# Kernel tuning notes

Hardware: AMD Instinct MI355X
Metric: run time of the kernel (lower is better)

The kernel has to match this reference:

```python
import jax, jax.numpy as jnp
import numpy as np

N, E, VD, HD, ES = 10000, 80000, 32, 64, 68
NET_IN = VD * VD + 2 * HD + ES   # 1220: f2s(1024) + s[e0](64) + s[e1](64) + edge_s(68)
SELF_IN = VD * VD + 2 * HD       # 1152: temp_f2s(1024) + s(64) + s_c(64)
OUT_D = VD * VD + HD             # 1088: vector channel mixer + scalar update


def _lecun(k, fin, fout):
    return jax.random.normal(k, (fin, fout), jnp.float32) / jnp.sqrt(jnp.float32(fin))


def setup_inputs() -> dict:
    ks = jax.random.split(jax.random.key(0), 16)
    return {
        "f": jax.random.normal(ks[0], (N, 3, VD), jnp.float32),
        "s": jax.random.normal(ks[1], (N, HD), jnp.float32),
        "edge_f": jax.random.normal(ks[2], (E, 3, 1), jnp.float32),
        "edge_s": jax.random.normal(ks[3], (E, ES), jnp.float32),
        "W_emb1": _lecun(ks[4], 2 * VD + 1, VD),
        "net_W1": _lecun(ks[5], NET_IN, HD), "net_b1": jnp.zeros((HD,), jnp.float32),
        "net_W2": _lecun(ks[6], HD, HD), "net_b2": jnp.zeros((HD,), jnp.float32),
        "net_W3": _lecun(ks[7], HD, OUT_D), "net_b3": jnp.zeros((OUT_D,), jnp.float32),
        "W_emb2": _lecun(ks[8], 2 * VD, VD),
        "self_W1": _lecun(ks[9], SELF_IN, HD), "self_b1": jnp.zeros((HD,), jnp.float32),
        "self_W2": _lecun(ks[10], HD, HD), "self_b2": jnp.zeros((HD,), jnp.float32),
        "self_W3": _lecun(ks[11], HD, OUT_D), "self_b3": jnp.zeros((OUT_D,), jnp.float32),
        "edge_index": jax.random.randint(ks[12], (2, E), 0, N),
    }


def _mlp(x, W1, b1, W2, b2, W3, b3):
    h = jax.nn.relu(x @ W1 + b1)
    h = jax.nn.relu(h @ W2 + b2)
    return h @ W3 + b3


def _segment_mean(x, ids, n):
    tot = jax.ops.segment_sum(x, ids, num_segments=n)
    cnt = jax.ops.segment_sum(jnp.ones(ids.shape, x.dtype), ids, num_segments=n)
    return tot / jnp.maximum(cnt, 1.0).reshape((n,) + (1,) * (x.ndim - 1))


def _forward(f, s, edge_f, edge_s,
             W_emb1, net_W1, net_b1, net_W2, net_b2, net_W3, net_b3,
             W_emb2, self_W1, self_b1, self_W2, self_b2, self_W3, self_b3,
             edge_index):
    n = f.shape[0]
    e0, e1 = edge_index[0], edge_index[1]
    # --- edge message: gather -> embed -> gram einsum -> MLP ---
    _f = jnp.concatenate((f[e0], f[e1], edge_f), axis=-1)          # [E,3,2VD+1]
    _s = jnp.concatenate((s[e0], s[e1], edge_s), axis=-1)          # [E,2HD+ES]
    _f = _f @ W_emb1                                               # [E,3,VD]
    f2s = jnp.einsum('eij,eik->ejk', _f, _f).reshape(-1, VD * VD)  # _f^T @ _f, [E,VD*VD]
    Fn = jnp.linalg.norm(f2s, axis=-1, keepdims=True) + 1.0
    c = _mlp(jnp.concatenate((f2s, _s), axis=-1),
             net_W1, net_b1, net_W2, net_b2, net_W3, net_b3) / Fn  # [E,OUT_D]
    f_c = jnp.einsum('eij,ejk->eik', _f, c[:, :VD * VD].reshape(-1, VD, VD))  # [E,3,VD]
    f_c = _segment_mean(f_c, e0, n)                                # [N,3,VD]
    s_c = _segment_mean(c[:, VD * VD:], e0, n)                     # [N,HD]
    # --- node self-update ---
    tf = jnp.concatenate((f, f_c), axis=-1) @ W_emb2               # [N,3,VD]
    tf2s = jnp.einsum('nij,nik->njk', tf, tf).reshape(n, VD * VD)
    Fn2 = jnp.linalg.norm(tf2s, axis=-1, keepdims=True) + 1.0
    c2 = _mlp(jnp.concatenate((tf2s, s, s_c), axis=-1),
              self_W1, self_b1, self_W2, self_b2, self_W3, self_b3) / Fn2
    f_out = jnp.einsum('nij,njk->nik', tf, c2[:, :VD * VD].reshape(-1, VD, VD)) + f
    s_out = c2[:, VD * VD:] + s
    return f_out, s_out


def reference(f, s, edge_f, edge_s,
              W_emb1, net_W1, net_b1, net_W2, net_b2, net_W3, net_b3,
              W_emb2, self_W1, self_b1, self_W2, self_b2, self_W3, self_b3,
              edge_index):
    return _forward(f, s, edge_f, edge_s,
                    W_emb1, net_W1, net_b1, net_W2, net_b2, net_W3, net_b3,
                    W_emb2, self_W1, self_b1, self_W2, self_b2, self_W3, self_b3,
                    edge_index)
```

## Files before the change

kernel.cpp:

```cpp
#include <hip/hip_runtime.h>
#include <math.h>

#define NN 10000
#define NE 80000
#define SFH 102
#define SFB 98
#define SSB 66
#define STX 72
#define NTRI 528
#define SAE 104
#define SAN 72

typedef __attribute__((ext_vector_type(8))) __bf16 bf16x8;
typedef __attribute__((ext_vector_type(8))) short short8v;
typedef __attribute__((ext_vector_type(4))) float f32x4;
typedef __attribute__((ext_vector_type(4))) unsigned uint4v;

__device__ __forceinline__ ushort f2bf(float x) {
  union { float f; unsigned u; } v; v.f = x;
  unsigned r = v.u + 0x7FFFu + ((v.u >> 16) & 1u);
  return (ushort)(r >> 16);
}
__device__ __forceinline__ float bfu(ushort u) {
  union { unsigned x; float f; } v; v.x = (unsigned)u << 16;
  return v.f;
}
__device__ __forceinline__ void tri_ab(int k, int& a, int& b) {
  int aa = 0, rem = k;
  while (rem >= 32 - aa) { rem -= 32 - aa; ++aa; }
  a = aa; b = aa + rem;
}

__global__ __launch_bounds__(1024)
void sgnn_scan(const int* __restrict__ deg, int* __restrict__ cursor,
               int* __restrict__ start) {
  __shared__ int sm[1024];
  const int t = threadIdx.x;
  const int i0 = t * 10;
  int v[10], pre = 0;
  #pragma unroll
  for (int q = 0; q < 10; ++q) {
    const int i = i0 + q;
    v[q] = (i < NN) ? deg[i] : 0;
    pre += v[q];
  }
  sm[t] = pre;
  __syncthreads();
  int run = pre;
  #pragma unroll
  for (int d = 1; d < 1024; d <<= 1) {
    const int add = (t >= d) ? sm[t - d] : 0;
    __syncthreads();
    run += add;
    sm[t] = run;
    __syncthreads();
  }
  int excl = run - pre;
  #pragma unroll
  for (int q = 0; q < 10; ++q) {
    const int i = i0 + q;
    if (i < NN) { cursor[i] = excl; start[i] = excl; }
    excl += v[q];
  }
}

__global__ __launch_bounds__(256)
void sgnn_scatter(const int* __restrict__ eidx, int* __restrict__ cursor,
                  int* __restrict__ sorted) {
  const int e = blockIdx.x * 256 + threadIdx.x;
  if (e < NE) {
    const int p = atomicAdd(cursor + eidx[e], 1);
    sorted[p] = e;
  }
}

__global__ __launch_bounds__(256)
void sgnn_wconv(const float* __restrict__ nW1, const float* __restrict__ nW2,
                const float* __restrict__ nW3, const float* __restrict__ sW1,
                const float* __restrict__ sW2, const float* __restrict__ sW3,
                const float* __restrict__ Wemb1, const float* __restrict__ Wemb2,
                const int* __restrict__ eidx, int* __restrict__ deg,
                ushort* __restrict__ wout, ushort* __restrict__ tab) {
  const int gid = blockIdx.x * 256 + threadIdx.x;
  if (gid < NE) atomicAdd(deg + eidx[gid], 1);
  if (gid >= 61 * 4096) {
    const int k = gid - 61 * 4096;
    if (k < NTRI) {
      int a, b; tri_ab(k, a, b);
      tab[k] = (ushort)(a | (b << 8) | ((a != b) ? 0x8000 : 0));
    }
    return;
  }
  const int tile = gid >> 12, idx = gid & 4095;
  const int c = idx >> 6, k = idx & 63;
  float v = 0.f;
  if (tile < 12) {
    const int T = tile;
    if (T < 8 || (T == 8 && k < 16)) {
      const int ktri = T * 64 + k;
      if (ktri < NTRI) {
        int a, b; tri_ab(ktri, a, b);
        v = nW1[(a * 32 + b) * 64 + c];
        if (a != b) v += nW1[(b * 32 + a) * 64 + c];
      }
    } else if (T == 8) { if (k < 20) v = nW1[(1216 + (k - 16)) * 64 + c]; }
    else if (T == 9)   v = nW1[(1024 + k) * 64 + c];
    else if (T == 10)  v = nW1[(1088 + k) * 64 + c];
    else               v = nW1[(1152 + k) * 64 + c];
  } else if (tile == 12) v = nW2[k * 64 + c];
  else if (tile < 30)    v = nW3[k * 1088 + (tile - 13) * 64 + c];
  else if (tile < 41) {
    const int T = tile - 30;
    if (T < 8 || (T == 8 && k < 16)) {
      const int ktri = T * 64 + k;
      if (ktri < NTRI) {
        int a, b; tri_ab(ktri, a, b);
        v = sW1[(a * 32 + b) * 64 + c];
        if (a != b) v += sW1[(b * 32 + a) * 64 + c];
      }
    } else if (T == 9) v = sW1[(1024 + k) * 64 + c];
    else if (T == 10)  v = sW1[(1088 + k) * 64 + c];
  } else if (tile == 41) v = sW2[k * 64 + c];
  else if (tile < 59)    v = sW3[k * 1088 + (tile - 42) * 64 + c];
  else if (tile == 59) {
    const int col = idx / 96, kk = idx % 96;
    v = (col < 32 && kk < 65) ? Wemb1[kk * 32 + col] : 0.f;
  } else {
    const int col = idx >> 6;
    v = (col < 32) ? Wemb2[k * 32 + col] : 0.f;
  }
  wout[gid] = f2bf(v);
}

#define WPRE_LOAD(srcbase) do { const ushort* _s = (srcbase);                    \
  wpre0 = *(const short8v*)&_s[(t >> 3) * 64 + (t & 7) * 8];                     \
  wpre1 = *(const short8v*)&_s[(32 + (t >> 3)) * 64 + (t & 7) * 8]; } while (0)

#define WPRE_STORE_TO(Wd) do { ushort* _d = (Wd);                                \
  *(short8v*)&_d[(t >> 3) * STX + (t & 7) * 8] = wpre0;                          \
  *(short8v*)&_d[(32 + (t >> 3)) * STX + (t & 7) * 8] = wpre1; } while (0)

#define MFMA_K64_RA_B(Wb) do { const ushort* _wl = (Wb);                         \
  acc[0] = __builtin_amdgcn_mfma_f32_16x16x32_bf16(af0.v8,                       \
      *(const bf16x8*)&_wl[(     ll) * STX + lh * 8], acc[0], 0, 0, 0);          \
  acc[1] = __builtin_amdgcn_mfma_f32_16x16x32_bf16(af0.v8,                       \
      *(const bf16x8*)&_wl[(16 + ll) * STX + lh * 8], acc[1], 0, 0, 0);          \
  acc[2] = __builtin_amdgcn_mfma_f32_16x16x32_bf16(af0.v8,                       \
      *(const bf16x8*)&_wl[(32 + ll) * STX + lh * 8], acc[2], 0, 0, 0);          \
  acc[3] = __builtin_amdgcn_mfma_f32_16x16x32_bf16(af0.v8,                       \
      *(const bf16x8*)&_wl[(48 + ll) * STX + lh * 8], acc[3], 0, 0, 0);          \
  acc[0] = __builtin_amdgcn_mfma_f32_16x16x32_bf16(af1.v8,                       \
      *(const bf16x8*)&_wl[(     ll) * STX + 32 + lh * 8], acc[0], 0, 0, 0);     \
  acc[1] = __builtin_amdgcn_mfma_f32_16x16x32_bf16(af1.v8,                       \
      *(const bf16x8*)&_wl[(16 + ll) * STX + 32 + lh * 8], acc[1], 0, 0, 0);     \
  acc[2] = __builtin_amdgcn_mfma_f32_16x16x32_bf16(af1.v8,                       \
      *(const bf16x8*)&_wl[(32 + ll) * STX + 32 + lh * 8], acc[2], 0, 0, 0);     \
  acc[3] = __builtin_amdgcn_mfma_f32_16x16x32_bf16(af1.v8,                       \
      *(const bf16x8*)&_wl[(48 + ll) * STX + 32 + lh * 8], acc[3], 0, 0, 0);     \
} while (0)

#define MFMA_K64_B(Xb, Wb) do { const ushort* _x = (Xb); const ushort* _wl = (Wb);\
  _Pragma("unroll") for (int kb = 0; kb < 2; ++kb) {                             \
    const bf16x8 af_ = *(const bf16x8*)&_x[(w * 16 + ll) * STX + kb * 32 + lh * 8]; \
    acc[0] = __builtin_amdgcn_mfma_f32_16x16x32_bf16(af_,                        \
        *(const bf16x8*)&_wl[(     ll) * STX + kb * 32 + lh * 8], acc[0], 0, 0, 0); \
    acc[1] = __builtin_amdgcn_mfma_f32_16x16x32_bf16(af_,                        \
        *(const bf16x8*)&_wl[(16 + ll) * STX + kb * 32 + lh * 8], acc[1], 0, 0, 0); \
    acc[2] = __builtin_amdgcn_mfma_f32_16x16x32_bf16(af_,                        \
        *(const bf16x8*)&_wl[(32 + ll) * STX + kb * 32 + lh * 8], acc[2], 0, 0, 0); \
    acc[3] = __builtin_amdgcn_mfma_f32_16x16x32_bf16(af_,                        \
        *(const bf16x8*)&_wl[(48 + ll) * STX + kb * 32 + lh * 8], acc[3], 0, 0, 0); \
  } } while (0)

#define ZERO_ACC() do { _Pragma("unroll") for (int q = 0; q < 4; ++q)            \
    acc[q] = (f32x4){0.f, 0.f, 0.f, 0.f}; } while (0)

#define PACK_STORE16(dstp) do {                                                  \
  unsigned pk[8];                                                                \
  _Pragma("unroll") for (int q = 0; q < 8; ++q)                                  \
    pk[q] = (unsigned)f2bf(xv[2 * q]) | ((unsigned)f2bf(xv[2 * q + 1]) << 16);   \
  *(uint4v*)(dstp)       = (uint4v){pk[0], pk[1], pk[2], pk[3]};                 \
  *(uint4v*)((dstp) + 8) = (uint4v){pk[4], pk[5], pk[6], pk[7]};                 \
} while (0)

#define PACK_AF() do {                                                           \
  _Pragma("unroll") for (int q2 = 0; q2 < 4; ++q2) {                             \
    af0.u[q2] = (unsigned)f2bf(xv[2 * q2]) | ((unsigned)f2bf(xv[2 * q2 + 1]) << 16); \
    af1.u[q2] = (unsigned)f2bf(xv[8 + 2 * q2]) | ((unsigned)f2bf(xv[8 + 2 * q2 + 1]) << 16); \
  } } while (0)

#define TRI8(kt, off) do {                                                       \
  int prev_a = -1; float fa0 = 0.f, fa1 = 0.f, fa2 = 0.f;                        \
  _Pragma("unroll") for (int q = 0; q < 8; ++q) {                                \
    const int tb = tabL[(kt) + q];                                               \
    const int a_ = tb & 31, b_ = (tb >> 8) & 31;                                 \
    if (a_ != prev_a) { fa0 = bfu(frA[a_]); fa1 = bfu(frA[32 + a_]);             \
                        fa2 = bfu(frA[64 + a_]); prev_a = a_; }                  \
    const float v = fmaf(fa0, bfu(frA[b_]),                                      \
        fmaf(fa1, bfu(frA[32 + b_]), fa2 * bfu(frA[64 + b_])));                  \
    const float wsel = (tb & 0x8000) ? 2.f : 1.f;                                \
    sumsq = fmaf(v * wsel, v, sumsq);                                            \
    xv[(off) + q] = v;                                                           \
  } } while (0)

#define XV8_LOAD(p, off) do { const float* _p = (p);                             \
  const float4 va = *(const float4*)(_p);                                        \
  const float4 vb = *(const float4*)(_p + 4);                                    \
  xv[(off)+0]=va.x; xv[(off)+1]=va.y; xv[(off)+2]=va.z; xv[(off)+3]=va.w;        \
  xv[(off)+4]=vb.x; xv[(off)+5]=vb.y; xv[(off)+6]=vb.z; xv[(off)+7]=vb.w;        \
} while (0)

#define XV_LOAD16(p) do { const float* _p = (p);                                 \
  _Pragma("unroll") for (int q = 0; q < 4; ++q) {                                \
    const float4 v4 = *(const float4*)(_p + 4 * q);                              \
    xv[4 * q + 0] = v4.x; xv[4 * q + 1] = v4.y;                                  \
    xv[4 * q + 2] = v4.z; xv[4 * q + 3] = v4.w; } } while (0)

#define CONSUME_NT() do {                                                        \
  _Pragma("unroll") for (int r = 0; r < 4; ++r) {                                \
    const int row_ = w * 16 + lh * 4 + r;                                        \
    const unsigned u0 = *(const unsigned*)&smFh[row_ * SFH +      nt * 2];       \
    const unsigned u1 = *(const unsigned*)&smFh[row_ * SFH + 32 + nt * 2];       \
    const unsigned u2 = *(const unsigned*)&smFh[row_ * SFH + 64 + nt * 2];       \
    union { unsigned x; float f; } l0, h0, l1, h1, l2, h2;                       \
    l0.x = u0 << 16; h0.x = u0 & 0xffff0000u;                                    \
    l1.x = u1 << 16; h1.x = u1 & 0xffff0000u;                                    \
    l2.x = u2 << 16; h2.x = u2 & 0xffff0000u;                                    \
    _Pragma("unroll") for (int nc = 0; nc < 4; ++nc) {                           \
      const float cv = (acc[nc][r] + b3v[nc]) * ifnr[r];                         \
      const int p = nc & 1;                                                      \
      const float f0 = (nc < 2) ? l0.f : h0.f;                                   \
      const float f1 = (nc < 2) ? l1.f : h1.f;                                   \
      const float f2 = (nc < 2) ? l2.f : h2.f;                                   \
      fch[(r * 3 + 0) * 2 + p] = fmaf(f0, cv, fch[(r * 3 + 0) * 2 + p]);         \
      fch[(r * 3 + 1) * 2 + p] = fmaf(f1, cv, fch[(r * 3 + 1) * 2 + p]);         \
      fch[(r * 3 + 2) * 2 + p] = fmaf(f2, cv, fch[(r * 3 + 2) * 2 + p]);         \
    }                                                                            \
  } } while (0)

#define STAGE_FS() do {                                                          \
  _Pragma("unroll") for (int r = 0; r < 4; ++r) {                                \
    const int row_ = w * 16 + lh * 4 + r;                                        \
    _Pragma("unroll") for (int i = 0; i < 3; ++i) {                              \
      F[row_ * SFB + i * 32 + ll]      = f2bf(fch[(r * 3 + i) * 2 + 0]);         \
      F[row_ * SFB + i * 32 + ll + 16] = f2bf(fch[(r * 3 + i) * 2 + 1]);         \
    }                                                                            \
    _Pragma("unroll") for (int nc = 0; nc < 4; ++nc)                             \
      S[row_ * SSB + nc * 16 + ll] = f2bf(cs[nc * 4 + r]);                       \
  } } while (0)

#define LDS_BYTES 43872

__global__ __launch_bounds__(256, 3)
void sgnn_edge(const float* __restrict__ f, const float* __restrict__ s,
               const float* __restrict__ edge_f, const float* __restrict__ edge_s,
               const float* __restrict__ b1, const float* __restrict__ b2,
               const float* __restrict__ b3,
               const ushort* __restrict__ wbf, const ushort* __restrict__ tab_g,
               const int* __restrict__ eidx, const int* __restrict__ sorted,
               const int* __restrict__ start_g, const int* __restrict__ deg_g,
               float* __restrict__ fc_sum, float* __restrict__ sc_sum) {
  __shared__ __align__(16) char sbuf[LDS_BYTES];
  ushort* smFh = (ushort*)sbuf;
  ushort* F    = (ushort*)sbuf;
  ushort* Xl   = (ushort*)(sbuf + 13056);
  ushort* S    = (ushort*)(sbuf + 13056);
  ushort* Aemb = (ushort*)(sbuf + 13056);
  ushort* Wl   = (ushort*)(sbuf + 22272);
  int*    snode = (int*)(sbuf + 31488);
  int*    srow0 = snode + 8;
  int*    srow1 = snode + 16;
  int*    sst   = snode + 24;
  int*    sdg   = snode + 32;
  ushort* tabL = (ushort*)(sbuf + 33088);
  float*  iFn  = (float*)(sbuf + 33088);
  int*    es_s = (int*)(sbuf + 34144);
  ushort* e0s  = (ushort*)(sbuf + 34400);
  ushort* e1s  = (ushort*)(sbuf + 34528);
  ushort* Wl1  = (ushort*)(sbuf + 34656);

  const int t = threadIdx.x, j = t & 63, w = t >> 6, eb = w * 16;
  const int lh = j >> 4, ll = j & 15;
  const int bid = blockIdx.x;
  const ushort* wembT = wbf + 59 * 4096;
  short8v wpre0, wpre1;

  if (t < 64) {
    const int e = sorted[bid * 64 + t];
    es_s[t] = e;
    e0s[t] = (ushort)eidx[e];
    e1s[t] = (ushort)eidx[NE + e];
  }
  for (int idx = t; idx < NTRI; idx += 256) tabL[idx] = tab_g[idx];
  __syncthreads();

  int str = 0, dgr = 0;
  if (j < 16) {
    const int n_ = e0s[eb + j];
    str = start_g[n_];
    dgr = deg_g[n_];
  }
  WPRE_LOAD(wbf + 0);

  #pragma unroll 1
  for (int h = 0; h < 2; ++h) {
    const int hb = h * 32;
    #pragma unroll 1
    for (int cc = t; cc < 576; cc += 256) {
      const int row = cc / 6, seg = cc - row * 6;
      const int lel = (row * 43) >> 7, il = row - lel * 3;
      const int k0 = seg * 16;
      float xv[16];
      if (seg < 4) {
        const int nd = (seg < 2) ? (int)e0s[hb + lel] : (int)e1s[hb + lel];
        XV_LOAD16(f + nd * 96 + il * 32 + (seg & 1) * 16);
      } else if (seg == 4) {
        xv[0] = edge_f[es_s[hb + lel] * 3 + il];
        #pragma unroll
        for (int m = 1; m < 16; ++m) xv[m] = 0.f;
      } else {
        #pragma unroll
        for (int m = 0; m < 16; ++m) xv[m] = 0.f;
      }
      PACK_STORE16(&Aemb[row * SAE + k0]);
    }
    __syncthreads();
    #pragma unroll 1
    for (int job = w * 3; job < w * 3 + 3; ++job) {
      const int mt = job >> 1, nt = job & 1;
      f32x4 ac = (f32x4){0.f, 0.f, 0.f, 0.f};
      #pragma unroll
      for (int kb = 0; kb < 3; ++kb) {
        const bf16x8 av = *(const bf16x8*)&Aemb[(mt * 16 + ll) * SAE + kb * 32 + lh * 8];
        const bf16x8 bv = *(const bf16x8*)&wembT[(nt * 16 + ll) * 96 + kb * 32 + lh * 8];
        ac = __builtin_amdgcn_mfma_f32_16x16x32_bf16(av, bv, ac, 0, 0, 0);
      }
      #pragma unroll
      for (int r = 0; r < 4; ++r) {
        const int rr = mt * 16 + lh * 4 + r;
        const int lel = (rr * 43) >> 7, il = rr - lel * 3;
        smFh[(hb + lel) * SFH + il * 32 + nt * 16 + ll] = f2bf(ac[r]);
      }
    }
    __syncthreads();
  }

  f32x4 acc[4];
  ZERO_ACC();
  float sumsq = 0.f;
  const int rowA = w * 16 + ll;
  const ushort* frA = smFh + rowA * SFH;

  WPRE_STORE_TO(Wl);
  WPRE_LOAD(wbf + 1 * 4096);
  __syncthreads();
  #pragma unroll 1
  for (int T = 0; T < 12; ++T) {
    ushort* Wc = (T & 1) ? Xl : Wl;
    ushort* Wn = (T & 1) ? Wl : Xl;
    float xv[16];
    union { unsigned u[4]; bf16x8 v8; } af0, af1;
    if (T < 8) {
      TRI8(T * 64 + lh * 8, 0);
      TRI8(T * 64 + 32 + lh * 8, 8);
    } else if (T == 8) {
      #pragma unroll
      for (int kb2 = 0; kb2 < 2; ++kb2)
        #pragma unroll
        for (int q = 0; q < 8; ++q) {
          const int k = kb2 * 32 + lh * 8 + q;
          float v = 0.f;
          if (k < 16) {
            const int tb = tabL[512 + k];
            const int a_ = tb & 31, b_ = (tb >> 8) & 31;
            v = fmaf(bfu(frA[a_]), bfu(frA[b_]),
                fmaf(bfu(frA[32 + a_]), bfu(frA[32 + b_]),
                     bfu(frA[64 + a_]) * bfu(frA[64 + b_])));
            const float wsel = (tb & 0x8000) ? 2.f : 1.f;
            sumsq = fmaf(v * wsel, v, sumsq);
          } else if (k < 20) {
            v = edge_s[es_s[rowA] * 68 + 64 + (k - 16)];
          }
          xv[kb2 * 8 + q] = v;
        }
    } else {
      const float* p = (T == 9)  ? (s + e0s[rowA] * 64)
                     : (T == 10) ? (s + e1s[rowA] * 64)
                                 : (edge_s + es_s[rowA] * 68);
      XV8_LOAD(p + lh * 8, 0);
      XV8_LOAD(p + 32 + lh * 8, 8);
    }
    PACK_AF();
    WPRE_STORE_TO(Wn);
    WPRE_LOAD(wbf + (T + 2) * 4096);
    MFMA_K64_RA_B(Wc);
    __syncthreads();
  }

  {
    float ss = sumsq;
    ss += __shfl_xor(ss, 16);
    ss += __shfl_xor(ss, 32);
    if (j < 16) iFn[eb + j] = 1.f / (sqrtf(ss) + 1.f);
  }
  #pragma unroll
  for (int nc = 0; nc < 4; ++nc) {
    const float bv = b1[nc * 16 + ll];
    #pragma unroll
    for (int r = 0; r < 4; ++r)
      Xl[(w * 16 + lh * 4 + r) * STX + nc * 16 + ll] = f2bf(fmaxf(acc[nc][r] + bv, 0.f));
  }
  ZERO_ACC();
  MFMA_K64_B(Xl, Wl);
  #pragma unroll
  for (int nc = 0; nc < 4; ++nc) {
    const float bv = b2[nc * 16 + ll];
    #pragma unroll
    for (int r = 0; r < 4; ++r)
      Xl[(w * 16 + lh * 4 + r) * STX + nc * 16 + ll] = f2bf(fmaxf(acc[nc][r] + bv, 0.f));
  }
  WPRE_STORE_TO(Wl1);
  WPRE_LOAD(wbf + 14 * 4096);
  __syncthreads();

  float fch[24];
  #pragma unroll
  for (int q = 0; q < 24; ++q) fch[q] = 0.f;
  float cs[16];
  float ifnr[4];
  #pragma unroll
  for (int r = 0; r < 4; ++r) ifnr[r] = iFn[w * 16 + lh * 4 + r];

  #pragma unroll 1
  for (int nt = 0; nt < 17; ++nt) {
    ushort* Wc = (nt & 1) ? Wl : Wl1;
    ushort* Wn = (nt & 1) ? Wl1 : Wl;
    if (nt < 16) {
      WPRE_STORE_TO(Wn);
      if (nt < 15) WPRE_LOAD(wbf + (15 + nt) * 4096);
    }
    float b3v[4];
    #pragma unroll
    for (int nc = 0; nc < 4; ++nc) b3v[nc] = b3[nt * 64 + nc * 16 + ll];
    ZERO_ACC();
    MFMA_K64_B(Xl, Wc);
    if (nt < 16) {
      CONSUME_NT();
    } else {
      #pragma unroll
      for (int nc = 0; nc < 4; ++nc)
        #pragma unroll
        for (int r = 0; r < 4; ++r)
          cs[nc * 4 + r] = (acc[nc][r] + b3v[nc]) * ifnr[r];
    }
    __syncthreads();
  }

  STAGE_FS();
  if (t < 8) snode[t] = -1;
  __syncthreads();

  {
    float r0 = 0.f, r1 = 0.f, rs = 0.f;
    int runlen = 0;
    const int gwb = bid * 64 + eb;
    #pragma unroll 1
    for (int m = 0; m < 16; ++m) {
      const int row = eb + m;
      r0 += bfu(F[row * SFB + j]);
      if (j < 32) r1 += bfu(F[row * SFB + 64 + j]);
      rs += bfu(S[row * SSB + j]);
      ++runlen;
      const int n = e0s[row];
      if (m == 15 || e0s[row + 1] != n) {
        const int st = __shfl(str, m);
        const int dg = __shfl(dgr, m);
        const int g1v = gwb + m, g0v = g1v - runlen + 1;
        if (g0v == st && runlen == dg) {
          fc_sum[n * 96 + j] = r0;
          if (j < 32) fc_sum[n * 96 + 64 + j] = r1;
          sc_sum[n * 64 + j] = rs;
        } else {
          const int slot = (g0v == gwb) ? 2 * w : 2 * w + 1;
          if (j == 0) {
            snode[slot] = n; srow0[slot] = row - runlen + 1; srow1[slot] = row;
            sst[slot] = st; sdg[slot] = dg;
          }
        }
        r0 = r1 = rs = 0.f; runlen = 0;
      }
    }
  }
  __syncthreads();

  if (t < 160) {
    const int ch = t;
    int prevn = -1;
    #pragma unroll 1
    for (int ss = 0; ss < 8; ++ss) {
      const int n = snode[ss];
      if (n < 0) continue;
      if (n != prevn) {
        float v = 0.f;
        #pragma unroll 1
        for (int k2 = ss; k2 < 8; ++k2) {
          if (snode[k2] == n) {
            #pragma unroll 1
            for (int row = srow0[k2]; row <= srow1[k2]; ++row)
              v += (ch < 96) ? bfu(F[row * SFB + ch]) : bfu(S[row * SSB + (ch - 96)]);
          } else if (k2 > ss && snode[k2] >= 0) break;
        }
        const bool cib = (sst[ss] >= bid * 64) && (sst[ss] + sdg[ss] <= bid * 64 + 64);
        float* dst = (ch < 96) ? (fc_sum + n * 96 + ch) : (sc_sum + n * 64 + (ch - 96));
        if (cib) *dst = v; else atomicAdd(dst, v);
      }
      prevn = n;
    }
  }
}

__global__ __launch_bounds__(256, 3)
void sgnn_node(const float* __restrict__ f, const float* __restrict__ s,
               const float* __restrict__ b1, const float* __restrict__ b2,
               const float* __restrict__ b3,
               const ushort* __restrict__ wbf, const ushort* __restrict__ tab_g,
               const float* __restrict__ fcm, const float* __restrict__ scm,
               const int* __restrict__ deg_g,
               float* __restrict__ of, float* __restrict__ os) {
  __shared__ __align__(16) char sbuf[LDS_BYTES];
  ushort* smFh = (ushort*)sbuf;
  ushort* F    = (ushort*)sbuf;
  ushort* Xl   = (ushort*)(sbuf + 13056);
  ushort* S    = (ushort*)(sbuf + 13056);
  ushort* Aemb = (ushort*)(sbuf + 13056);
  ushort* Wl   = (ushort*)(sbuf + 22272);
  float*  icntL = (float*)(sbuf + 31488);
  ushort* tabL = (ushort*)(sbuf + 33088);
  float*  iFn  = (float*)(sbuf + 33088);
  ushort* Wl1  = (ushort*)(sbuf + 34656);

  const int t = threadIdx.x, j = t & 63, w = t >> 6, eb = w * 16;
  const int lh = j >> 4, ll = j & 15;
  const int nbase = blockIdx.x * 64;
  const ushort* wembTn = wbf + 60 * 4096;
  short8v wpre0, wpre1;

  for (int idx = t; idx < NTRI; idx += 256) tabL[idx] = tab_g[idx];
  if (t < 64)
    icntL[t] = 1.f / fmaxf((float)deg_g[min(nbase + t, NN - 1)], 1.f);
  WPRE_LOAD(wbf + 30 * 4096);
  __syncthreads();

  #pragma unroll 1
  for (int h = 0; h < 2; ++h) {
    const int hb = h * 32;
    #pragma unroll 1
    for (int cc = t; cc < 384; cc += 256) {
      const int row = cc >> 2, seg = cc & 3;
      const int lel = (row * 43) >> 7, il = row - lel * 3;
      const int nc = min(nbase + hb + lel, NN - 1);
      const int k0 = seg * 16;
      float xv[16];
      if (seg < 2) {
        XV_LOAD16(f + nc * 96 + il * 32 + seg * 16);
      } else {
        XV_LOAD16(fcm + nc * 96 + il * 32 + (seg - 2) * 16);
        const float ic = icntL[hb + lel];
        #pragma unroll
        for (int m = 0; m < 16; ++m) xv[m] *= ic;
      }
      PACK_STORE16(&Aemb[row * SAN + k0]);
    }
    __syncthreads();
    #pragma unroll 1
    for (int job = w * 3; job < w * 3 + 3; ++job) {
      const int mt = job >> 1, nt = job & 1;
      f32x4 ac = (f32x4){0.f, 0.f, 0.f, 0.f};
      #pragma unroll
      for (int kb = 0; kb < 2; ++kb) {
        const bf16x8 av = *(const bf16x8*)&Aemb[(mt * 16 + ll) * SAN + kb * 32 + lh * 8];
        const bf16x8 bv = *(const bf16x8*)&wembTn[(nt * 16 + ll) * 64 + kb * 32 + lh * 8];
        ac = __builtin_amdgcn_mfma_f32_16x16x32_bf16(av, bv, ac, 0, 0, 0);
      }
      #pragma unroll
      for (int r = 0; r < 4; ++r) {
        const int rr = mt * 16 + lh * 4 + r;
        const int lel = (rr * 43) >> 7, il = rr - lel * 3;
        smFh[(hb + lel) * SFH + il * 32 + nt * 16 + ll] = f2bf(ac[r]);
      }
    }
    __syncthreads();
  }

  f32x4 acc[4];
  ZERO_ACC();
  float sumsq = 0.f;
  const int rowA = w * 16 + ll;
  const ushort* frA = smFh + rowA * SFH;
  const int ncA = min(nbase + rowA, NN - 1);

  WPRE_STORE_TO(Xl);
  WPRE_LOAD(wbf + 31 * 4096);
  __syncthreads();
  #pragma unroll 1
  for (int T = 0; T < 11; ++T) {
    ushort* Wc = (T & 1) ? Wl : Xl;
    ushort* Wn = (T & 1) ? Xl : Wl;
    float xv[16];
    union { unsigned u[4]; bf16x8 v8; } af0, af1;
    if (T < 8) {
      TRI8(T * 64 + lh * 8, 0);
      TRI8(T * 64 + 32 + lh * 8, 8);
    } else if (T == 8) {
      #pragma unroll
      for (int kb2 = 0; kb2 < 2; ++kb2)
        #pragma unroll
        for (int q = 0; q < 8; ++q) {
          const int k = kb2 * 32 + lh * 8 + q;
          float v = 0.f;
          if (k < 16) {
            const int tb = tabL[512 + k];
            const int a_ = tb & 31, b_ = (tb >> 8) & 31;
            v = fmaf(bfu(frA[a_]), bfu(frA[b_]),
                fmaf(bfu(frA[32 + a_]), bfu(frA[32 + b_]),
                     bfu(frA[64 + a_]) * bfu(frA[64 + b_])));
            const float wsel = (tb & 0x8000) ? 2.f : 1.f;
            sumsq = fmaf(v * wsel, v, sumsq);
          }
          xv[kb2 * 8 + q] = v;
        }
    } else if (T == 9) {
      XV8_LOAD(s + ncA * 64 + lh * 8, 0);
      XV8_LOAD(s + ncA * 64 + 32 + lh * 8, 8);
    } else {
      const float ic = icntL[rowA];
      XV8_LOAD(scm + ncA * 64 + lh * 8, 0);
      XV8_LOAD(scm + ncA * 64 + 32 + lh * 8, 8);
      #pragma unroll
      for (int m = 0; m < 16; ++m) xv[m] *= ic;
    }
    PACK_AF();
    WPRE_STORE_TO(Wn);
    WPRE_LOAD(wbf + (32 + T) * 4096);
    MFMA_K64_RA_B(Wc);
    __syncthreads();
  }

  {
    float ss = sumsq;
    ss += __shfl_xor(ss, 16);
    ss += __shfl_xor(ss, 32);
    if (j < 16) iFn[eb + j] = 1.f / (sqrtf(ss) + 1.f);
  }
  #pragma unroll
  for (int nc = 0; nc < 4; ++nc) {
    const float bv = b1[nc * 16 + ll];
    #pragma unroll
    for (int r = 0; r < 4; ++r)
      Xl[(w * 16 + lh * 4 + r) * STX + nc * 16 + ll] = f2bf(fmaxf(acc[nc][r] + bv, 0.f));
  }
  ZERO_ACC();
  MFMA_K64_B(Xl, Wl);
  #pragma unroll
  for (int nc = 0; nc < 4; ++nc) {
    const float bv = b2[nc * 16 + ll];
    #pragma unroll
    for (int r = 0; r < 4; ++r)
      Xl[(w * 16 + lh * 4 + r) * STX + nc * 16 + ll] = f2bf(fmaxf(acc[nc][r] + bv, 0.f));
  }
  WPRE_STORE_TO(Wl1);
  WPRE_LOAD(wbf + 43 * 4096);
  __syncthreads();

  float fch[24];
  #pragma unroll
  for (int q = 0; q < 24; ++q) fch[q] = 0.f;
  float cs[16];
  float ifnr[4];
  #pragma unroll
  for (int r = 0; r < 4; ++r) ifnr[r] = iFn[w * 16 + lh * 4 + r];

  #pragma unroll 1
  for (int nt = 0; nt < 17; ++nt) {
    ushort* Wc = (nt & 1) ? Wl : Wl1;
    ushort* Wn = (nt & 1) ? Wl1 : Wl;
    if (nt < 16) {
      WPRE_STORE_TO(Wn);
      if (nt < 15) WPRE_LOAD(wbf + (44 + nt) * 4096);
    }
    float b3v[4];
    #pragma unroll
    for (int nc = 0; nc < 4; ++nc) b3v[nc] = b3[nt * 64 + nc * 16 + ll];
    ZERO_ACC();
    MFMA_K64_B(Xl, Wc);
    if (nt < 16) {
      CONSUME_NT();
    } else {
      #pragma unroll
      for (int nc = 0; nc < 4; ++nc)
        #pragma unroll
        for (int r = 0; r < 4; ++r)
          cs[nc * 4 + r] = (acc[nc][r] + b3v[nc]) * ifnr[r];
    }
    __syncthreads();
  }

  STAGE_FS();
  __syncthreads();

  #pragma unroll 1
  for (int m = 0; m < 16; ++m) {
    const int row = eb + m;
    const int n_m = nbase + row;
    if (n_m < NN) {
      of[n_m * 96 + j] = bfu(F[row * SFB + j]) + f[n_m * 96 + j];
      if (j < 32)
        of[n_m * 96 + 64 + j] = bfu(F[row * SFB + 64 + j]) + f[n_m * 96 + 64 + j];
      os[n_m * 64 + j] = bfu(S[row * SSB + j]) + s[n_m * 64 + j];
    }
  }
}

extern "C" void kernel_launch(void* const* d_in, const int* in_sizes, int n_in,
                              void* d_out, int out_size, void* d_ws, size_t ws_size,
                              hipStream_t stream) {
  const float* f      = (const float*)d_in[0];
  const float* s      = (const float*)d_in[1];
  const float* edge_f = (const float*)d_in[2];
  const float* edge_s = (const float*)d_in[3];
  const float* Wemb1  = (const float*)d_in[4];
  const float* nW1 = (const float*)d_in[5];
  const float* nb1 = (const float*)d_in[6];
  const float* nW2 = (const float*)d_in[7];
  const float* nb2 = (const float*)d_in[8];
  const float* nW3 = (const float*)d_in[9];
  const float* nb3 = (const float*)d_in[10];
  const float* Wemb2 = (const float*)d_in[11];
  const float* sW1 = (const float*)d_in[12];
  const float* sb1 = (const float*)d_in[13];
  const float* sW2 = (const float*)d_in[14];
  const float* sb2 = (const float*)d_in[15];
  const float* sW3 = (const float*)d_in[16];
  const float* sb3 = (const float*)d_in[17];
  const int* eidx  = (const int*)d_in[18];

  float* of = (float*)d_out;
  float* os = of + (size_t)NN * 96;

  int* deg    = (int*)d_ws;
  int* cursor = deg + NN;
  int* start  = cursor + NN;
  int* sorted = start + NN;
  ushort* wbf = (ushort*)(sorted + NE);
  ushort* tab = wbf + 61 * 4096;

  hipMemsetAsync(deg, 0, (size_t)NN * 4, stream);
  hipMemsetAsync(d_out, 0, (size_t)NN * 160 * 4, stream);

  hipLaunchKernelGGL(sgnn_wconv, dim3((61 * 4096 + NTRI + 255) / 256), dim3(256),
                     0, stream, nW1, nW2, nW3, sW1, sW2, sW3, Wemb1, Wemb2,
                     eidx, deg, wbf, tab);
  hipLaunchKernelGGL(sgnn_scan, dim3(1), dim3(1024), 0, stream, deg, cursor, start);
  hipLaunchKernelGGL(sgnn_scatter, dim3((NE + 255) / 256), dim3(256), 0, stream,
                     eidx, cursor, sorted);
  hipLaunchKernelGGL(sgnn_edge, dim3(NE / 64), dim3(256), 0, stream,
                     f, s, edge_f, edge_s, nb1, nb2, nb3,
                     wbf, tab, eidx, sorted, start, deg,
                     of , os );
  hipLaunchKernelGGL(sgnn_node, dim3((NN + 63) / 64), dim3(256), 0, stream,
                     f, s, sb1, sb2, sb3,
                     wbf, tab, of , os , deg, of, os);
}
```

Baseline: 195.1 us.

## Shrink node kernel blocks to 32 nodes with 128 threads

The node-update kernel now handles 32 nodes per block with 2 waves instead of 64 nodes with 4 waves. This doubles the grid to about 313 blocks so more CUs get work, and roughly halves LDS per block. Weight staging changes from register prefetch one tile ahead to direct global-to-LDS copies into double-buffered LDS. In exchange, each weight tile is loaded by twice as many blocks, and the load latency is no longer hidden behind the previous tile's MFMA work.

```diff
diff --git a/kernel.cpp b/kernel.cpp
--- a/kernel.cpp
+++ b/kernel.cpp
@@ -140,6 +140,12 @@
   *(short8v*)&_d[(t >> 3) * STX + (t & 7) * 8] = wpre0;                          \
   *(short8v*)&_d[(32 + (t >> 3)) * STX + (t & 7) * 8] = wpre1; } while (0)
 
+#define NSTAGE_W(Wd, srcbase) do { ushort* _d = (Wd); const ushort* _s = (srcbase);\
+  _Pragma("unroll") for (int rr = 0; rr < 4; ++rr) {                             \
+    const int idx_ = t + 128 * rr; const int c_ = idx_ >> 3, ko_ = idx_ & 7;     \
+    *(short8v*)&_d[c_ * STX + ko_ * 8] = *(const short8v*)&_s[c_ * 64 + ko_ * 8];\
+  } } while (0)
+
 #define MFMA_K64_RA_B(Wb) do { const ushort* _wl = (Wb);                         \
   acc[0] = __builtin_amdgcn_mfma_f32_16x16x32_bf16(af0.v8,                       \
       *(const bf16x8*)&_wl[(     ll) * STX + lh * 8], acc[0], 0, 0, 0);          \
@@ -519,7 +525,9 @@
   }
 }
 
-__global__ __launch_bounds__(256, 3)
+#define NLDS_BYTES 30752
+
+__global__ __launch_bounds__(128, 2)
 void sgnn_node(const float* __restrict__ f, const float* __restrict__ s,
                const float* __restrict__ b1, const float* __restrict__ b2,
                const float* __restrict__ b3,
@@ -527,70 +535,64 @@
                const float* __restrict__ fcm, const float* __restrict__ scm,
                const int* __restrict__ deg_g,
                float* __restrict__ of, float* __restrict__ os) {
-  __shared__ __align__(16) char sbuf[LDS_BYTES];
+  __shared__ __align__(16) char sbuf[NLDS_BYTES];
   ushort* smFh = (ushort*)sbuf;
   ushort* F    = (ushort*)sbuf;
-  ushort* Xl   = (ushort*)(sbuf + 13056);
-  ushort* S    = (ushort*)(sbuf + 13056);
-  ushort* Aemb = (ushort*)(sbuf + 13056);
-  ushort* Wl   = (ushort*)(sbuf + 22272);
-  float*  icntL = (float*)(sbuf + 31488);
-  ushort* tabL = (ushort*)(sbuf + 33088);
-  float*  iFn  = (float*)(sbuf + 33088);
-  ushort* Wl1  = (ushort*)(sbuf + 34656);
+  ushort* Xl   = (ushort*)(sbuf + 6528);
+  ushort* S    = (ushort*)(sbuf + 6528);
+  ushort* Aemb = (ushort*)(sbuf + 6528);
+  ushort* Wl   = (ushort*)(sbuf + 11136);
+  ushort* Wl1  = (ushort*)(sbuf + 20352);
+  float*  icntL = (float*)(sbuf + 29568);
+  ushort* tabL = (ushort*)(sbuf + 29696);
+  float*  iFn  = (float*)(sbuf + 29696);
 
   const int t = threadIdx.x, j = t & 63, w = t >> 6, eb = w * 16;
   const int lh = j >> 4, ll = j & 15;
-  const int nbase = blockIdx.x * 64;
+  const int nbase = blockIdx.x * 32;
   const ushort* wembTn = wbf + 60 * 4096;
-  short8v wpre0, wpre1;
-
-  for (int idx = t; idx < NTRI; idx += 256) tabL[idx] = tab_g[idx];
-  if (t < 64)
+
+  for (int idx = t; idx < NTRI; idx += 128) tabL[idx] = tab_g[idx];
+  if (t < 32)
     icntL[t] = 1.f / fmaxf((float)deg_g[min(nbase + t, NN - 1)], 1.f);
-  WPRE_LOAD(wbf + 30 * 4096);
   __syncthreads();
 
   #pragma unroll 1
-  for (int h = 0; h < 2; ++h) {
-    const int hb = h * 32;
-    #pragma unroll 1
-    for (int cc = t; cc < 384; cc += 256) {
-      const int row = cc >> 2, seg = cc & 3;
-      const int lel = (row * 43) >> 7, il = row - lel * 3;
-      const int nc = min(nbase + hb + lel, NN - 1);
-      const int k0 = seg * 16;
-      float xv[16];
-      if (seg < 2) {
-        XV_LOAD16(f + nc * 96 + il * 32 + seg * 16);
-      } else {
-        XV_LOAD16(fcm + nc * 96 + il * 32 + (seg - 2) * 16);
-        const float ic = icntL[hb + lel];
-        #pragma unroll
-        for (int m = 0; m < 16; ++m) xv[m] *= ic;
-      }
-      PACK_STORE16(&Aemb[row * SAN + k0]);
-    }
-    __syncthreads();
-    #pragma unroll 1
-    for (int job = w * 3; job < w * 3 + 3; ++job) {
-      const int mt = job >> 1, nt = job & 1;
-      f32x4 ac = (f32x4){0.f, 0.f, 0.f, 0.f};
+  for (int cc = t; cc < 384; cc += 128) {
+    const int row = cc >> 2, seg = cc & 3;
+    const int lel = (row * 43) >> 7, il = row - lel * 3;
+    const int nc = min(nbase + lel, NN - 1);
+    const int k0 = seg * 16;
+    float xv[16];
+    if (seg < 2) {
+      XV_LOAD16(f + nc * 96 + il * 32 + seg * 16);
+    } else {
+      XV_LOAD16(fcm + nc * 96 + il * 32 + (seg - 2) * 16);
+      const float ic = icntL[lel];
       #pragma unroll
-      for (int kb = 0; kb < 2; ++kb) {
-        const bf16x8 av = *(const bf16x8*)&Aemb[(mt * 16 + ll) * SAN + kb * 32 + lh * 8];
-        const bf16x8 bv = *(const bf16x8*)&wembTn[(nt * 16 + ll) * 64 + kb * 32 + lh * 8];
-        ac = __builtin_amdgcn_mfma_f32_16x16x32_bf16(av, bv, ac, 0, 0, 0);
-      }
-      #pragma unroll
-      for (int r = 0; r < 4; ++r) {
-        const int rr = mt * 16 + lh * 4 + r;
-        const int lel = (rr * 43) >> 7, il = rr - lel * 3;
-        smFh[(hb + lel) * SFH + il * 32 + nt * 16 + ll] = f2bf(ac[r]);
-      }
-    }
-    __syncthreads();
-  }
+      for (int m = 0; m < 16; ++m) xv[m] *= ic;
+    }
+    PACK_STORE16(&Aemb[row * SAN + k0]);
+  }
+  __syncthreads();
+  #pragma unroll 1
+  for (int job = w * 6; job < w * 6 + 6; ++job) {
+    const int mt = job >> 1, nt = job & 1;
+    f32x4 ac = (f32x4){0.f, 0.f, 0.f, 0.f};
+    #pragma unroll
+    for (int kb = 0; kb < 2; ++kb) {
+      const bf16x8 av = *(const bf16x8*)&Aemb[(mt * 16 + ll) * SAN + kb * 32 + lh * 8];
+      const bf16x8 bv = *(const bf16x8*)&wembTn[(nt * 16 + ll) * 64 + kb * 32 + lh * 8];
+      ac = __builtin_amdgcn_mfma_f32_16x16x32_bf16(av, bv, ac, 0, 0, 0);
+    }
+    #pragma unroll
+    for (int r = 0; r < 4; ++r) {
+      const int rr = mt * 16 + lh * 4 + r;
+      const int lel = (rr * 43) >> 7, il = rr - lel * 3;
+      smFh[lel * SFH + il * 32 + nt * 16 + ll] = f2bf(ac[r]);
+    }
+  }
+  __syncthreads();
 
   f32x4 acc[4];
   ZERO_ACC();
@@ -599,13 +601,12 @@
   const ushort* frA = smFh + rowA * SFH;
   const int ncA = min(nbase + rowA, NN - 1);
 
-  WPRE_STORE_TO(Xl);
-  WPRE_LOAD(wbf + 31 * 4096);
+  NSTAGE_W(Wl, wbf + 30 * 4096);
   __syncthreads();
   #pragma unroll 1
   for (int T = 0; T < 11; ++T) {
-    ushort* Wc = (T & 1) ? Wl : Xl;
-    ushort* Wn = (T & 1) ? Xl : Wl;
+    ushort* Wc = (T & 1) ? Wl1 : Wl;
+    ushort* Wn = (T & 1) ? Wl : Wl1;
     float xv[16];
     union { unsigned u[4]; bf16x8 v8; } af0, af1;
     if (T < 8) {
@@ -640,8 +641,7 @@
       for (int m = 0; m < 16; ++m) xv[m] *= ic;
     }
     PACK_AF();
-    WPRE_STORE_TO(Wn);
-    WPRE_LOAD(wbf + (32 + T) * 4096);
+    NSTAGE_W(Wn, wbf + (31 + T) * 4096);
     MFMA_K64_RA_B(Wc);
     __syncthreads();
   }
@@ -660,7 +660,7 @@
       Xl[(w * 16 + lh * 4 + r) * STX + nc * 16 + ll] = f2bf(fmaxf(acc[nc][r] + bv, 0.f));
   }
   ZERO_ACC();
-  MFMA_K64_B(Xl, Wl);
+  MFMA_K64_B(Xl, Wl1);
   #pragma unroll
   for (int nc = 0; nc < 4; ++nc) {
     const float bv = b2[nc * 16 + ll];
@@ -668,8 +668,7 @@
     for (int r = 0; r < 4; ++r)
       Xl[(w * 16 + lh * 4 + r) * STX + nc * 16 + ll] = f2bf(fmaxf(acc[nc][r] + bv, 0.f));
   }
-  WPRE_STORE_TO(Wl1);
-  WPRE_LOAD(wbf + 43 * 4096);
+  NSTAGE_W(Wl, wbf + 42 * 4096);
   __syncthreads();
 
   float fch[24];
@@ -682,12 +681,9 @@
 
   #pragma unroll 1
   for (int nt = 0; nt < 17; ++nt) {
-    ushort* Wc = (nt & 1) ? Wl : Wl1;
-    ushort* Wn = (nt & 1) ? Wl1 : Wl;
-    if (nt < 16) {
-      WPRE_STORE_TO(Wn);
-      if (nt < 15) WPRE_LOAD(wbf + (44 + nt) * 4096);
-    }
+    ushort* Wc = (nt & 1) ? Wl1 : Wl;
+    ushort* Wn = (nt & 1) ? Wl : Wl1;
+    if (nt < 16) NSTAGE_W(Wn, wbf + (43 + nt) * 4096);
     float b3v[4];
     #pragma unroll
     for (int nc = 0; nc < 4; ++nc) b3v[nc] = b3[nt * 64 + nc * 16 + ll];
@@ -767,7 +763,7 @@
                      f, s, edge_f, edge_s, nb1, nb2, nb3,
                      wbf, tab, eidx, sorted, start, deg,
                      of , os );
-  hipLaunchKernelGGL(sgnn_node, dim3((NN + 63) / 64), dim3(256), 0, stream,
+  hipLaunchKernelGGL(sgnn_node, dim3((NN + 31) / 32), dim3(128), 0, stream,
                      f, s, sb1, sb2, sb3,
                      wbf, tab, of , os , deg, of, os);
 }
```

New measurement: 198.5 us. No clear change (+1.8%).
